# Kernel optimization log

Hardware: AMD Instinct MI355X
Metric: run time of the kernel (lower is better)

Reference implementation:

```python
import jax, jax.numpy as jnp
import numpy as np

EMBED_DIM = 1024
NUM_HEADS = 16
HEAD_DIM = EMBED_DIM // NUM_HEADS


def setup_inputs() -> dict:
    key = jax.random.key(0)
    k1, k2, k3 = jax.random.split(key, 3)
    B, S = 2, 2048
    x = jax.random.normal(k1, (B, S, EMBED_DIM), dtype=jnp.float32)
    # Xavier-uniform-style init for dense kernels
    lim_qkv = float(np.sqrt(6.0 / (EMBED_DIM + 3 * EMBED_DIM)))
    w_qkv = jax.random.uniform(k2, (EMBED_DIM, 3 * EMBED_DIM), jnp.float32, -lim_qkv, lim_qkv)
    b_qkv = jnp.zeros((3 * EMBED_DIM,), jnp.float32)
    lim_out = float(np.sqrt(6.0 / (EMBED_DIM + EMBED_DIM)))
    w_out = jax.random.uniform(k3, (EMBED_DIM, EMBED_DIM), jnp.float32, -lim_out, lim_out)
    b_out = jnp.zeros((EMBED_DIM,), jnp.float32)
    return {"x": x, "w_qkv": w_qkv, "b_qkv": b_qkv, "w_out": w_out, "b_out": b_out}


def reference(x, w_qkv, b_qkv, w_out, b_out):
    B, S, E = x.shape
    qkv = x @ w_qkv + b_qkv                       # [B, S, 3E]
    qkv = qkv.reshape(B, S, NUM_HEADS, 3 * HEAD_DIM)
    qkv = qkv.transpose(0, 2, 1, 3)               # [B, H, S, 3*dh]
    q, k, v = jnp.split(qkv, 3, axis=-1)          # each [B, H, S, dh]
    scale = 1.0 / jnp.sqrt(jnp.asarray(HEAD_DIM, x.dtype))
    logits = jnp.einsum('bhqd,bhkd->bhqk', q, k) * scale  # [B, H, S, S]
    attn = jax.nn.softmax(logits, axis=-1)
    vals = jnp.einsum('bhqk,bhkd->bhqd', attn, v)  # [B, H, S, dh]
    vals = vals.transpose(0, 2, 1, 3).reshape(B, S, E)
    return vals @ w_out + b_out
```

## Files before the change

### kernel.cpp

```cpp
#include <hip/hip_runtime.h>
#include <cstdint>

typedef unsigned short u16;
typedef unsigned int u32;
typedef __attribute__((ext_vector_type(8))) short bf16x8;
typedef __attribute__((ext_vector_type(4))) float f32x4;
typedef __attribute__((ext_vector_type(16))) float f32x16;
typedef __attribute__((ext_vector_type(2))) unsigned int u32x2;

#if __has_builtin(__builtin_amdgcn_exp2f)
#define EXP2(x) __builtin_amdgcn_exp2f(x)
#else
#define EXP2(x) exp2f(x)
#endif

__device__ __forceinline__ u16 f2bf(float f) {
  unsigned u = __float_as_uint(f);
  u += 0x7fffu + ((u >> 16) & 1u);
  return (u16)(u >> 16);
}
__device__ __forceinline__ u32 pk_bf16(float lo, float hi) {
#if __has_builtin(__builtin_amdgcn_cvt_pk_bf16_f32)
  auto r = __builtin_amdgcn_cvt_pk_bf16_f32(lo, hi);
  return __builtin_bit_cast(u32, r);
#else
  u32 a = __float_as_uint(lo), b = __float_as_uint(hi);
  a += 0x7fffu + ((a >> 16) & 1u);
  b += 0x7fffu + ((b >> 16) & 1u);
  return (a >> 16) | (b & 0xffff0000u);
#endif
}

__device__ __forceinline__ void plane32swap(u32 x, u32 y, u32& r0, u32& r1) {
#if __has_builtin(__builtin_amdgcn_permlane32_swap)
  u32x2 r = __builtin_amdgcn_permlane32_swap(x, y, false, false);
  r0 = r[0]; r1 = r[1];
#else
  const u32 xs = (u32)__shfl_xor((int)x, 32, 64);
  const u32 ys = (u32)__shfl_xor((int)y, 32, 64);
  const bool hi = (threadIdx.x & 32) != 0;
  r0 = hi ? ys : x;
  r1 = hi ? y : xs;
#endif
}

__device__ __forceinline__ void async_load16(const void* g, void* l) {
  typedef const __attribute__((address_space(1))) void* gp_t;
  typedef __attribute__((address_space(3))) void* lp_t;
  __builtin_amdgcn_global_load_lds((gp_t)(uintptr_t)g, (lp_t)(uintptr_t)l, 16, 0, 0);
}

__global__ __launch_bounds__(256) void preprocess(
    const float* __restrict__ x, u16* __restrict__ xb,
    const float* __restrict__ wqkv, u16* __restrict__ dqkv,
    const float* __restrict__ wout, u16* __restrict__ dout)
{
  __shared__ u16 tile[64][65];
  const int t = threadIdx.x;
  const int bx = blockIdx.x;
  if (bx < 2048) {
    const size_t i = ((size_t)bx * 256 + t) * 8;
    const float4 a = *(const float4*)(x + i);
    const float4 b = *(const float4*)(x + i + 4);
    union { u16 u[8]; bf16x8 v; } p;
    p.u[0] = f2bf(a.x); p.u[1] = f2bf(a.y); p.u[2] = f2bf(a.z); p.u[3] = f2bf(a.w);
    p.u[4] = f2bf(b.x); p.u[5] = f2bf(b.y); p.u[6] = f2bf(b.z); p.u[7] = f2bf(b.w);
    *(bf16x8*)(xb + i) = p.v;
    return;
  }
  const int tb = bx - 2048;
  const int bxx = tb & 63, byy = tb >> 6;
  const bool isOut = bxx >= 48;
  const float* src = isOut ? wout : wqkv;
  u16* dst = isOut ? dout : dqkv;
  const int cols = isOut ? 1024 : 3072;
  const int rows = 1024;
  const int tc = (isOut ? (bxx - 48) : bxx) * 64;
  const int tr = byy * 64;
  const int r = t >> 2, c0 = (t & 3) * 16;
  const float* sp = src + (size_t)(tr + r) * cols + tc + c0;
#pragma unroll
  for (int i = 0; i < 16; i += 4) {
    const float4 v = *(const float4*)(sp + i);
    tile[r][c0 + i + 0] = f2bf(v.x);
    tile[r][c0 + i + 1] = f2bf(v.y);
    tile[r][c0 + i + 2] = f2bf(v.z);
    tile[r][c0 + i + 3] = f2bf(v.w);
  }
  __syncthreads();
  u16* dp = dst + (size_t)(tc + r) * rows + tr + c0;
#pragma unroll
  for (int i = 0; i < 16; ++i) dp[i] = tile[c0 + i][r];
}

__global__ __launch_bounds__(256) void gemm_qkv(
    const u16* __restrict__ A, const u16* __restrict__ Bt, const float* __restrict__ bias,
    u16* __restrict__ Qp, u16* __restrict__ Kp, u16* __restrict__ Vtp)
{
  const int Kd = 1024;
  __shared__ __align__(16) u16 As[2][128 * 32];
  __shared__ __align__(16) u16 Bs[2][128 * 32];
  const int t = threadIdx.x;
  const int lane = t & 63, wave = t >> 6;
  const int quad = lane >> 4, m16 = lane & 15;
  const int mb = blockIdx.y * 128, nb = blockIdx.x * 128;
  const int wr = (wave & 1) * 64, wc = (wave >> 1) * 64;

  const int seg = (nb + wc) >> 6;
  const int h = seg / 3;
  const int which = seg - 3 * h;
  const bool isV = (which == 2);

  const int srow = t >> 2;
  const int scol = (t & 3) * 8;
  const u16* Ag0 = A + (size_t)(mb + srow) * Kd + scol;
  const u16* Ag1 = Ag0 + (size_t)64 * Kd;
  const u16* Bg0 = Bt + (size_t)(nb + srow) * Kd + scol;
  const u16* Bg1 = Bg0 + (size_t)64 * Kd;
  const int aoff = t * 8;

  f32x4 acc[4][4] = {};

#define GPRE(k0, B)                                                          \
  do {                                                                       \
    async_load16(Ag0 + (k0), &As[B][aoff]);                                  \
    async_load16(Ag1 + (k0), &As[B][aoff + 2048]);                           \
    async_load16(Bg0 + (k0), &Bs[B][aoff]);                                  \
    async_load16(Bg1 + (k0), &Bs[B][aoff + 2048]);                           \
  } while (0)

#define GSTEP(B)                                                             \
  do {                                                                       \
    bf16x8 af[4], bfr[4];                                                    \
    _Pragma("unroll")                                                        \
    for (int i = 0; i < 4; ++i)                                              \
      af[i] = *(const bf16x8*)(&As[B][(wr + i * 16 + m16) * 32 + quad * 8]); \
    _Pragma("unroll")                                                        \
    for (int i = 0; i < 4; ++i)                                              \
      bfr[i] = *(const bf16x8*)(&Bs[B][(wc + i * 16 + m16) * 32 + quad * 8]); \
    if (isV) {                                                               \
      _Pragma("unroll")                                                      \
      for (int i = 0; i < 4; ++i)                                            \
        _Pragma("unroll")                                                    \
        for (int j = 0; j < 4; ++j)                                          \
          acc[i][j] = __builtin_amdgcn_mfma_f32_16x16x32_bf16(bfr[i], af[j], acc[i][j], 0, 0, 0); \
    } else {                                                                 \
      _Pragma("unroll")                                                      \
      for (int i = 0; i < 4; ++i)                                            \
        _Pragma("unroll")                                                    \
        for (int j = 0; j < 4; ++j)                                          \
          acc[i][j] = __builtin_amdgcn_mfma_f32_16x16x32_bf16(af[i], bfr[j], acc[i][j], 0, 0, 0); \
    }                                                                        \
  } while (0)

  GPRE(0, 0);
  __syncthreads();
  for (int k0 = 0; k0 < Kd; k0 += 64) {
    GPRE(k0 + 32, 1);
    GSTEP(0);
    __syncthreads();
    if (k0 + 64 < Kd) GPRE(k0 + 64, 0);
    GSTEP(1);
    __syncthreads();
  }
#undef GPRE
#undef GSTEP

  const int b = mb >> 11;
  const size_t bh64 = (size_t)((b << 4) | h);

  if (isV) {
    const int sIbase = (mb & 2047) + wr;
    u16* dstV = Vtp + bh64 * 64 * 2048;
#pragma unroll
    for (int i = 0; i < 4; ++i)
#pragma unroll
      for (int r = 0; r < 4; ++r) {
        const int d = i * 16 + quad * 4 + r;
        const float bv = bias[nb + wc + d];
        u16* rp = dstV + (size_t)d * 2048 + sIbase;
#pragma unroll
        for (int j = 0; j < 4; ++j)
          rp[j * 16 + m16] = f2bf(acc[i][j][r] + bv);
      }
  } else {
    u16* dstP = (which == 0) ? Qp : Kp;
    const float qs = (which == 0) ? 0.18033688011112042f : 1.0f;
#pragma unroll
    for (int j = 0; j < 4; ++j) {
      const int base = nb + wc + j * 16;
      const float bv = bias[base + m16];
      const int d = (base & 63) + m16;
#pragma unroll
      for (int i = 0; i < 4; ++i)
#pragma unroll
        for (int r = 0; r < 4; ++r) {
          const int row = mb + wr + i * 16 + quad * 4 + r;
          const int sI = row & 2047;
          dstP[(bh64 * 2048 + sI) * 64 + d] = f2bf((acc[i][j][r] + bv) * qs);
        }
    }
  }
}

__global__ __launch_bounds__(256) void gemm_out(
    const u16* __restrict__ A, const u16* __restrict__ Bt, const float* __restrict__ bias,
    float* __restrict__ Outp)
{
  const int Kd = 1024;
  __shared__ __align__(16) u16 As[2][64 * 32];
  __shared__ __align__(16) u16 Bs[2][128 * 32];
  const int t = threadIdx.x;
  const int lane = t & 63, wave = t >> 6;
  const int quad = lane >> 4, m16 = lane & 15;
  const int mb = blockIdx.y * 64, nb = blockIdx.x * 128;
  const int wr = (wave & 1) * 32, wc = (wave >> 1) * 64;

  const int srow = t >> 2;
  const int scol = (t & 3) * 8;
  const u16* Ag0 = A + (size_t)(mb + srow) * Kd + scol;
  const u16* Bg0 = Bt + (size_t)(nb + srow) * Kd + scol;
  const u16* Bg1 = Bg0 + (size_t)64 * Kd;
  const int aoff = t * 8;

  f32x4 acc[2][4] = {};

#define OPRE(k0, B)                                                          \
  do {                                                                       \
    async_load16(Ag0 + (k0), &As[B][aoff]);                                  \
    async_load16(Bg0 + (k0), &Bs[B][aoff]);                                  \
    async_load16(Bg1 + (k0), &Bs[B][aoff + 2048]);                           \
  } while (0)

#define OSTEP(B)                                                             \
  do {                                                                       \
    bf16x8 af[2], bfr[4];                                                    \
    _Pragma("unroll")                                                        \
    for (int i = 0; i < 2; ++i)                                              \
      af[i] = *(const bf16x8*)(&As[B][(wr + i * 16 + m16) * 32 + quad * 8]); \
    _Pragma("unroll")                                                        \
    for (int j = 0; j < 4; ++j)                                              \
      bfr[j] = *(const bf16x8*)(&Bs[B][(wc + j * 16 + m16) * 32 + quad * 8]); \
    _Pragma("unroll")                                                        \
    for (int i = 0; i < 2; ++i)                                              \
      _Pragma("unroll")                                                      \
      for (int j = 0; j < 4; ++j)                                            \
        acc[i][j] = __builtin_amdgcn_mfma_f32_16x16x32_bf16(af[i], bfr[j], acc[i][j], 0, 0, 0); \
  } while (0)

  OPRE(0, 0);
  __syncthreads();
  for (int k0 = 0; k0 < Kd; k0 += 64) {
    OPRE(k0 + 32, 1);
    OSTEP(0);
    __syncthreads();
    if (k0 + 64 < Kd) OPRE(k0 + 64, 0);
    OSTEP(1);
    __syncthreads();
  }
#undef OPRE
#undef OSTEP

#pragma unroll
  for (int j = 0; j < 4; ++j) {
    const int col = nb + wc + j * 16 + m16;
    const float bv = bias[col];
#pragma unroll
    for (int i = 0; i < 2; ++i)
#pragma unroll
      for (int r = 0; r < 4; ++r) {
        const int row = mb + wr + i * 16 + quad * 4 + r;
        Outp[(size_t)row * 1024 + col] = acc[i][j][r] + bv;
      }
  }
}

__global__ __launch_bounds__(512) void flash_attn(
    const u16* __restrict__ Q, const u16* __restrict__ K, const u16* __restrict__ Vt,
    u16* __restrict__ O)
{
  const int S = 2048;
  __shared__ __align__(16) u16 SH[32768];
  u16* const KlF = SH;
  u16* const VlF = SH + 16384;
  const int t = threadIdx.x;
  const int lane = t & 63, w = t >> 6;
  const int l31 = lane & 31, hi = lane >> 5;
  const int wq = w & 3;
  const int half = w >> 2;
  const int hoff = half * 8192;

  const int f = blockIdx.x;
  const int wi = f >> 3;
  const int bh = (f & 7) + 8 * (wi & 3);
  const int q0 = (wi >> 2) * 128;

  const u16* Qb = Q + (size_t)bh * S * 64;
  const u16* Kb = K + (size_t)bh * S * 64;
  const u16* Vb = Vt + (size_t)bh * 64 * S;

  bf16x8 qf[4];
#pragma unroll
  for (int dc = 0; dc < 4; ++dc)
    qf[dc] = *(const bf16x8*)(Qb + (size_t)(q0 + wq * 32 + l31) * 64 + dc * 16 + hi * 8);

  const int tidx = t & 255;
  const u16* Kg[2]; const u16* Vg[2]; int soff[2];
#pragma unroll
  for (int l = 0; l < 2; ++l) {
    const int idx = l * 256 + tidx;
    const int row = idx >> 3, slot = idx & 7;
    const int sg = slot ^ (row & 7);
    Kg[l] = Kb + (size_t)(half * 1024 + row) * 64 + sg * 8;
    Vg[l] = Vb + (size_t)row * S + half * 1024 + sg * 8;
    soff[l] = idx * 8;
  }

  f32x16 ot[2] = {};
  float lr4[4] = {0.f, 0.f, 0.f, 0.f};

#define PRE(tile, B)                                                         \
  do {                                                                       \
    _Pragma("unroll")                                                        \
    for (int l = 0; l < 2; ++l)                                              \
      async_load16(Kg[l] + (size_t)(tile) * 4096, KlF + hoff + (B) * 4096 + soff[l]); \
    _Pragma("unroll")                                                        \
    for (int l = 0; l < 2; ++l)                                              \
      async_load16(Vg[l] + (tile) * 64, VlF + hoff + (B) * 4096 + soff[l]);  \
  } while (0)

#define STEP(B)                                                              \
  do {                                                                       \
    const u16* kb_ = KlF + hoff + (B) * 4096;                                \
    const u16* vb_ = VlF + hoff + (B) * 4096;                                \
    bf16x8 pa[4];                                                            \
    _Pragma("unroll")                                                        \
    for (int kt = 0; kt < 2; ++kt) {                                         \
      f32x16 st = {0.f,0.f,0.f,0.f, 0.f,0.f,0.f,0.f,                         \
                   0.f,0.f,0.f,0.f, 0.f,0.f,0.f,0.f};                        \
      const int kvr = kt * 32 + l31;                                         \
      const u16* krow = kb_ + kvr * 64;                                      \
      _Pragma("unroll")                                                      \
      for (int dc = 0; dc < 4; ++dc) {                                       \
        const bf16x8 kb = *(const bf16x8*)(krow + (((dc * 2 + hi) ^ (kvr & 7)) * 8)); \
        st = __builtin_amdgcn_mfma_f32_32x32x16_bf16(kb, qf[dc], st, 0, 0, 0); \
      }                                                                      \
      float p[16];                                                           \
      _Pragma("unroll")                                                      \
      for (int r = 0; r < 16; ++r) { p[r] = EXP2(st[r]); lr4[r & 3] += p[r]; } \
      _Pragma("unroll")                                                      \
      for (int cc = 0; cc < 2; ++cc) {                                       \
        union { u32 u[4]; bf16x8 v; } fr;                                    \
        _Pragma("unroll")                                                    \
        for (int i = 0; i < 2; ++i) {                                        \
          const u32 xx = pk_bf16(p[8 * cc + 2 * i + 0], p[8 * cc + 2 * i + 1]); \
          const u32 yy = pk_bf16(p[8 * cc + 2 * i + 4], p[8 * cc + 2 * i + 5]); \
          u32 r0, r1;                                                        \
          plane32swap(xx, yy, r0, r1);                                       \
          fr.u[i] = r0; fr.u[2 + i] = r1;                                    \
        }                                                                    \
        pa[kt * 2 + cc] = fr.v;                                              \
      }                                                                      \
    }                                                                        \
    _Pragma("unroll")                                                        \
    for (int c = 0; c < 4; ++c) {                                            \
      _Pragma("unroll")                                                      \
      for (int dt = 0; dt < 2; ++dt) {                                       \
        const int dr = dt * 32 + l31;                                        \
        const bf16x8 va = *(const bf16x8*)(vb_ + dr * 64 + (((c * 2 + hi) ^ (dr & 7)) * 8)); \
        ot[dt] = __builtin_amdgcn_mfma_f32_32x32x16_bf16(va, pa[c], ot[dt], 0, 0, 0); \
      }                                                                      \
    }                                                                        \
  } while (0)

  PRE(0, 0);
  __syncthreads();

  for (int tp = 0; tp < 16; tp += 2) {
    PRE(tp + 1, 1);
    STEP(0);
    __syncthreads();
    if (tp + 2 < 16) PRE(tp + 2, 0);
    STEP(1);
    __syncthreads();
  }
#undef PRE
#undef STEP

  float l = lr4[0] + lr4[1] + lr4[2] + lr4[3];
  l += __shfl_xor(l, 32, 64);

  float* const smemF = (float*)SH;
  if (half == 1) {
#pragma unroll
    for (int dt = 0; dt < 2; ++dt)
#pragma unroll
      for (int r = 0; r < 16; ++r)
        smemF[wq * 2112 + (dt * 16 + r) * 64 + lane] = ot[dt][r];
    smemF[wq * 2112 + 2048 + lane] = l;
  }
  __syncthreads();
  if (half == 0) {
    l += smemF[wq * 2112 + 2048 + lane];
#pragma unroll
    for (int dt = 0; dt < 2; ++dt)
#pragma unroll
      for (int r = 0; r < 16; ++r)
        ot[dt][r] += smemF[wq * 2112 + (dt * 16 + r) * 64 + lane];

    const float inv = 1.0f / l;
    const int b = bh >> 4, h = bh & 15;
    const int q = q0 + wq * 32 + l31;
    u16* base = O + ((size_t)b * 2048 + q) * 1024 + h * 64;
#pragma unroll
    for (int dt = 0; dt < 2; ++dt)
#pragma unroll
      for (int g4 = 0; g4 < 4; ++g4) {
        const u32 lo = pk_bf16(ot[dt][4 * g4 + 0] * inv, ot[dt][4 * g4 + 1] * inv);
        const u32 h2 = pk_bf16(ot[dt][4 * g4 + 2] * inv, ot[dt][4 * g4 + 3] * inv);
        *(uint2*)(base + dt * 32 + 8 * g4 + 4 * hi) = make_uint2(lo, h2);
      }
  }
}

extern "C" void kernel_launch(void* const* d_in, const int* in_sizes, int n_in,
                              void* d_out, int out_size, void* d_ws, size_t ws_size,
                              hipStream_t stream)
{
  const float* x     = (const float*)d_in[0];
  const float* w_qkv = (const float*)d_in[1];
  const float* b_qkv = (const float*)d_in[2];
  const float* w_out = (const float*)d_in[3];
  const float* b_out = (const float*)d_in[4];
  float* out = (float*)d_out;

  u16* ws     = (u16*)d_ws;
  u16* xb     = ws;
  u16* WtQKV  = xb + 4194304;
  u16* WtOut  = WtQKV + 3145728;
  u16* Qm     = WtOut + 1048576;
  u16* Km     = Qm + 4194304;
  u16* Vtm    = Km + 4194304;
  u16* AO     = Vtm + 4194304;

  preprocess<<<3072, 256, 0, stream>>>(x, xb, w_qkv, WtQKV, w_out, WtOut);
  gemm_qkv<<<dim3(24, 32), 256, 0, stream>>>(xb, WtQKV, b_qkv, Qm, Km, Vtm);
  flash_attn<<<512, 512, 0, stream>>>(Qm, Km, Vtm, AO);
  gemm_out<<<dim3(8, 64), 256, 0, stream>>>(AO, WtOut, b_out, out);
}
```

Before: 185.9 us.

## Process two query tiles per wave in flash attention to reuse K/V fragments

Each wave now computes 64 query rows (two 32-row tiles) against every K/V tile it loads from LDS, so each K and V fragment read feeds two MFMAs. The block covers 256 queries and the grid is halved to 256 blocks. The cross-half reduction buffer in shared memory is enlarged to hold both tiles' accumulators and row sums. This cuts LDS read traffic per unit of MFMA work, but it doubles accumulator and score registers, which may lower occupancy, and with half the blocks there is less parallelism to hide latency.

```diff
diff --git a/kernel.cpp b/kernel.cpp
--- a/kernel.cpp
+++ b/kernel.cpp
@@ -280,7 +280,7 @@
     u16* __restrict__ O)
 {
   const int S = 2048;
-  __shared__ __align__(16) u16 SH[32768];
+  __shared__ __align__(16) u16 SH[33792];
   u16* const KlF = SH;
   u16* const VlF = SH + 16384;
   const int t = threadIdx.x;
@@ -293,16 +293,18 @@
   const int f = blockIdx.x;
   const int wi = f >> 3;
   const int bh = (f & 7) + 8 * (wi & 3);
-  const int q0 = (wi >> 2) * 128;
+  const int q0 = (wi >> 2) * 256;
 
   const u16* Qb = Q + (size_t)bh * S * 64;
   const u16* Kb = K + (size_t)bh * S * 64;
   const u16* Vb = Vt + (size_t)bh * 64 * S;
 
-  bf16x8 qf[4];
-#pragma unroll
-  for (int dc = 0; dc < 4; ++dc)
-    qf[dc] = *(const bf16x8*)(Qb + (size_t)(q0 + wq * 32 + l31) * 64 + dc * 16 + hi * 8);
+  bf16x8 qf0[4], qf1[4];
+#pragma unroll
+  for (int dc = 0; dc < 4; ++dc) {
+    qf0[dc] = *(const bf16x8*)(Qb + (size_t)(q0 + wq * 64 + l31) * 64 + dc * 16 + hi * 8);
+    qf1[dc] = *(const bf16x8*)(Qb + (size_t)(q0 + wq * 64 + 32 + l31) * 64 + dc * 16 + hi * 8);
+  }
 
   const int tidx = t & 255;
   const u16* Kg[2]; const u16* Vg[2]; int soff[2];
@@ -316,8 +318,9 @@
     soff[l] = idx * 8;
   }
 
-  f32x16 ot[2] = {};
-  float lr4[4] = {0.f, 0.f, 0.f, 0.f};
+  f32x16 ot[2][2] = {};
+  float lr0[4] = {0.f, 0.f, 0.f, 0.f};
+  float lr1[4] = {0.f, 0.f, 0.f, 0.f};
 
 #define PRE(tile, B)                                                         \
   do {                                                                       \
@@ -333,21 +336,23 @@
   do {                                                                       \
     const u16* kb_ = KlF + hoff + (B) * 4096;                                \
     const u16* vb_ = VlF + hoff + (B) * 4096;                                \
-    bf16x8 pa[4];                                                            \
+    bf16x8 pa0[4], pa1[4];                                                   \
     _Pragma("unroll")                                                        \
     for (int kt = 0; kt < 2; ++kt) {                                         \
-      f32x16 st = {0.f,0.f,0.f,0.f, 0.f,0.f,0.f,0.f,                         \
+      f32x16 s0 = {0.f,0.f,0.f,0.f, 0.f,0.f,0.f,0.f,                         \
                    0.f,0.f,0.f,0.f, 0.f,0.f,0.f,0.f};                        \
+      f32x16 s1 = s0;                                                        \
       const int kvr = kt * 32 + l31;                                         \
       const u16* krow = kb_ + kvr * 64;                                      \
       _Pragma("unroll")                                                      \
       for (int dc = 0; dc < 4; ++dc) {                                       \
         const bf16x8 kb = *(const bf16x8*)(krow + (((dc * 2 + hi) ^ (kvr & 7)) * 8)); \
-        st = __builtin_amdgcn_mfma_f32_32x32x16_bf16(kb, qf[dc], st, 0, 0, 0); \
+        s0 = __builtin_amdgcn_mfma_f32_32x32x16_bf16(kb, qf0[dc], s0, 0, 0, 0); \
+        s1 = __builtin_amdgcn_mfma_f32_32x32x16_bf16(kb, qf1[dc], s1, 0, 0, 0); \
       }                                                                      \
       float p[16];                                                           \
       _Pragma("unroll")                                                      \
-      for (int r = 0; r < 16; ++r) { p[r] = EXP2(st[r]); lr4[r & 3] += p[r]; } \
+      for (int r = 0; r < 16; ++r) { p[r] = EXP2(s0[r]); lr0[r & 3] += p[r]; } \
       _Pragma("unroll")                                                      \
       for (int cc = 0; cc < 2; ++cc) {                                       \
         union { u32 u[4]; bf16x8 v; } fr;                                    \
@@ -359,7 +364,22 @@
           plane32swap(xx, yy, r0, r1);                                       \
           fr.u[i] = r0; fr.u[2 + i] = r1;                                    \
         }                                                                    \
-        pa[kt * 2 + cc] = fr.v;                                              \
+        pa0[kt * 2 + cc] = fr.v;                                             \
+      }                                                                      \
+      _Pragma("unroll")                                                      \
+      for (int r = 0; r < 16; ++r) { p[r] = EXP2(s1[r]); lr1[r & 3] += p[r]; } \
+      _Pragma("unroll")                                                      \
+      for (int cc = 0; cc < 2; ++cc) {                                       \
+        union { u32 u[4]; bf16x8 v; } fr;                                    \
+        _Pragma("unroll")                                                    \
+        for (int i = 0; i < 2; ++i) {                                        \
+          const u32 xx = pk_bf16(p[8 * cc + 2 * i + 0], p[8 * cc + 2 * i + 1]); \
+          const u32 yy = pk_bf16(p[8 * cc + 2 * i + 4], p[8 * cc + 2 * i + 5]); \
+          u32 r0, r1;                                                        \
+          plane32swap(xx, yy, r0, r1);                                       \
+          fr.u[i] = r0; fr.u[2 + i] = r1;                                    \
+        }                                                                    \
+        pa1[kt * 2 + cc] = fr.v;                                             \
       }                                                                      \
     }                                                                        \
     _Pragma("unroll")                                                        \
@@ -368,7 +388,8 @@
       for (int dt = 0; dt < 2; ++dt) {                                       \
         const int dr = dt * 32 + l31;                                        \
         const bf16x8 va = *(const bf16x8*)(vb_ + dr * 64 + (((c * 2 + hi) ^ (dr & 7)) * 8)); \
-        ot[dt] = __builtin_amdgcn_mfma_f32_32x32x16_bf16(va, pa[c], ot[dt], 0, 0, 0); \
+        ot[0][dt] = __builtin_amdgcn_mfma_f32_32x32x16_bf16(va, pa0[c], ot[0][dt], 0, 0, 0); \
+        ot[1][dt] = __builtin_amdgcn_mfma_f32_32x32x16_bf16(va, pa1[c], ot[1][dt], 0, 0, 0); \
       }                                                                      \
     }                                                                        \
   } while (0)
@@ -387,39 +408,52 @@
 #undef PRE
 #undef STEP
 
-  float l = lr4[0] + lr4[1] + lr4[2] + lr4[3];
-  l += __shfl_xor(l, 32, 64);
+  float l0 = lr0[0] + lr0[1] + lr0[2] + lr0[3];
+  float l1 = lr1[0] + lr1[1] + lr1[2] + lr1[3];
+  l0 += __shfl_xor(l0, 32, 64);
+  l1 += __shfl_xor(l1, 32, 64);
 
   float* const smemF = (float*)SH;
   if (half == 1) {
 #pragma unroll
-    for (int dt = 0; dt < 2; ++dt)
-#pragma unroll
-      for (int r = 0; r < 16; ++r)
-        smemF[wq * 2112 + (dt * 16 + r) * 64 + lane] = ot[dt][r];
-    smemF[wq * 2112 + 2048 + lane] = l;
+    for (int qt = 0; qt < 2; ++qt)
+#pragma unroll
+      for (int dt = 0; dt < 2; ++dt)
+#pragma unroll
+        for (int r = 0; r < 16; ++r)
+          smemF[wq * 4096 + (qt * 32 + dt * 16 + r) * 64 + lane] = ot[qt][dt][r];
+    smemF[16384 + wq * 128 + lane] = l0;
+    smemF[16384 + wq * 128 + 64 + (lane & 63) * 0 + lane] = l1;
   }
   __syncthreads();
   if (half == 0) {
-    l += smemF[wq * 2112 + 2048 + lane];
-#pragma unroll
-    for (int dt = 0; dt < 2; ++dt)
-#pragma unroll
-      for (int r = 0; r < 16; ++r)
-        ot[dt][r] += smemF[wq * 2112 + (dt * 16 + r) * 64 + lane];
-
-    const float inv = 1.0f / l;
+    l0 += smemF[16384 + wq * 128 + lane];
+    l1 += smemF[16384 + wq * 128 + 64 + lane];
+#pragma unroll
+    for (int qt = 0; qt < 2; ++qt)
+#pragma unroll
+      for (int dt = 0; dt < 2; ++dt)
+#pragma unroll
+        for (int r = 0; r < 16; ++r)
+          ot[qt][dt][r] += smemF[wq * 4096 + (qt * 32 + dt * 16 + r) * 64 + lane];
+
     const int b = bh >> 4, h = bh & 15;
-    const int q = q0 + wq * 32 + l31;
-    u16* base = O + ((size_t)b * 2048 + q) * 1024 + h * 64;
-#pragma unroll
-    for (int dt = 0; dt < 2; ++dt)
-#pragma unroll
-      for (int g4 = 0; g4 < 4; ++g4) {
-        const u32 lo = pk_bf16(ot[dt][4 * g4 + 0] * inv, ot[dt][4 * g4 + 1] * inv);
-        const u32 h2 = pk_bf16(ot[dt][4 * g4 + 2] * inv, ot[dt][4 * g4 + 3] * inv);
-        *(uint2*)(base + dt * 32 + 8 * g4 + 4 * hi) = make_uint2(lo, h2);
-      }
+    const float inv0 = 1.0f / l0;
+    const float inv1 = 1.0f / l1;
+#pragma unroll
+    for (int qt = 0; qt < 2; ++qt) {
+      const float inv = qt ? inv1 : inv0;
+      const int q = q0 + wq * 64 + qt * 32 + l31;
+      u16* base = O + ((size_t)b * 2048 + q) * 1024 + h * 64;
+#pragma unroll
+      for (int dt = 0; dt < 2; ++dt)
+#pragma unroll
+        for (int g4 = 0; g4 < 4; ++g4) {
+          const u32 lo = pk_bf16(ot[qt][dt][4 * g4 + 0] * inv, ot[qt][dt][4 * g4 + 1] * inv);
+          const u32 h2 = pk_bf16(ot[qt][dt][4 * g4 + 2] * inv, ot[qt][dt][4 * g4 + 3] * inv);
+          *(uint2*)(base + dt * 32 + 8 * g4 + 4 * hi) = make_uint2(lo, h2);
+        }
+    }
   }
 }
 
@@ -445,6 +479,6 @@
 
   preprocess<<<3072, 256, 0, stream>>>(x, xb, w_qkv, WtQKV, w_out, WtOut);
   gemm_qkv<<<dim3(24, 32), 256, 0, stream>>>(xb, WtQKV, b_qkv, Qm, Km, Vtm);
-  flash_attn<<<512, 512, 0, stream>>>(Qm, Km, Vtm, AO);
+  flash_attn<<<256, 512, 0, stream>>>(Qm, Km, Vtm, AO);
   gemm_out<<<dim3(8, 64), 256, 0, stream>>>(AO, WtOut, b_out, out);
 }
```

Result: faster. 181.6 us (-2.3%).
